# Performance work log

Measured on AMD Instinct MI355X. Metric: run time of the kernel, lower is better.

## Reference

```python
import jax, jax.numpy as jnp
import numpy as np

N, K, G = 4096, 4096, 128  # out_features, in_features, groupsize


def setup_inputs() -> dict:
    key = jax.random.key(0)
    k1, k2, k3, k4 = jax.random.split(key, 4)
    input = jax.random.normal(k1, (1, 2048, K), dtype=jnp.float32)
    # packed int4 weights: each byte holds two 4-bit codes (high nibble = even k, low = odd k)
    weight_packed = jax.random.randint(k2, (N, K // 2), 0, 256, dtype=jnp.int32)
    scales = jax.random.uniform(k3, (K // G, N), dtype=jnp.float32) * 0.02 + 1e-3
    zeros = jax.random.normal(k4, (K // G, N), dtype=jnp.float32) * 0.05
    scales_and_zeros = jnp.stack([scales, zeros], axis=-1)  # (K//G, N, 2)
    return {"input": input, "weight_packed": weight_packed,
            "scales_and_zeros": scales_and_zeros, "groupsize": G}


def reference(input, weight_packed, scales_and_zeros, groupsize):
    n, k_half = weight_packed.shape
    k = 2 * k_half
    g = k // groupsize
    # unpack two int4 codes per byte: high nibble first (even k index), then low nibble
    hi = (weight_packed >> 4) & 0xF
    lo = weight_packed & 0xF
    q = jnp.stack([hi, lo], axis=-1).reshape(n, k)  # (N, K), codes in [0,15]
    scales = scales_and_zeros[..., 0].T  # (N, G)
    zeros = scales_and_zeros[..., 1].T   # (N, G)
    # group-wise affine dequant: w = (q - 8) * scale + zero
    qg = q.reshape(n, g, groupsize).astype(jnp.float32)
    w = (qg - 8.0) * scales[:, :, None] + zeros[:, :, None]  # (N, G, gs)
    w = w.reshape(n, k)
    # out[..., n] = sum_k input[..., k] * w[n, k]
    return jnp.einsum('bsk,nk->bsn', input, w)
```

## Files before the change

kernel.cpp:

```cpp
#include <hip/hip_runtime.h>
#include <hip/hip_bf16.h>


using bf16x8 = __attribute__((ext_vector_type(8))) short;
using f32x16 = __attribute__((ext_vector_type(16))) float;

#define KK 4096
#define NN 4096
#define NT (KK / 64)

static __device__ __forceinline__ short f2bf(float f) {
    __hip_bfloat16 h = __float2bfloat16(f);
    return __builtin_bit_cast(short, h);
}

#define GLDS16(gptr, lptr) __builtin_amdgcn_global_load_lds( \
    (const __attribute__((address_space(1))) void*)(gptr),   \
    (__attribute__((address_space(3))) void*)(lptr), 16, 0, 0)

#define MFMA32 __builtin_amdgcn_mfma_f32_32x32x16_bf16

__global__ __launch_bounds__(256) void dequant_w(
    const int* __restrict__ W, const float* __restrict__ SZ,
    short* __restrict__ Wd)
{
    const int idx = blockIdx.x * 256 + threadIdx.x;
    const int n   = idx >> 9;
    const int q4  = idx & 511;
    const int kh0 = q4 << 2;
    const int g   = kh0 >> 6;
    const float2 sz = *(const float2*)(SZ + ((size_t)g * NN + n) * 2);
    const float scale = sz.x;
    const float zs    = sz.y - 8.0f * sz.x;
    int4 p = *(const int4*)(W + (size_t)n * (KK / 2) + kh0);
    int vals[4] = {p.x, p.y, p.z, p.w};
    bf16x8 r;
    #pragma unroll
    for (int j = 0; j < 4; ++j) {
        int v = vals[j];
        r[2 * j]     = f2bf((float)((v >> 4) & 0xF) * scale + zs);
        r[2 * j + 1] = f2bf((float)(v & 0xF) * scale + zs);
    }
    *(bf16x8*)&Wd[(size_t)n * KK + (kh0 << 1)] = r;
}

__global__ __launch_bounds__(256) void cvt_a(
    const float* __restrict__ A, short* __restrict__ Ab)
{
    const int idx = blockIdx.x * 256 + threadIdx.x;
    const float4* s = (const float4*)(A + (size_t)idx * 8);
    float4 u = s[0], v = s[1];
    bf16x8 r;
    r[0] = f2bf(u.x); r[1] = f2bf(u.y); r[2] = f2bf(u.z); r[3] = f2bf(u.w);
    r[4] = f2bf(v.x); r[5] = f2bf(v.y); r[6] = f2bf(v.z); r[7] = f2bf(v.w);
    *(bf16x8*)&Ab[(size_t)idx * 8] = r;
}

__global__ __launch_bounds__(512, 2) void gemm_pl(
    const short* __restrict__ Ab, const short* __restrict__ Bb,
    float* __restrict__ C)
{
    __shared__ short sA[3 * 256 * 64];
    __shared__ short sB[3 * 128 * 64];

    const int tid  = threadIdx.x;
    const int lane = tid & 63;
    const int wave = tid >> 6;
    const int wm   = wave >> 1;
    const int wn   = wave & 1;
    const int bm   = blockIdx.y * 256;
    const int bn   = blockIdx.x * 128;

    const int sl = lane >> 3;
    const int sc = (lane & 7) ^ sl;
    const short* aSt = Ab + (size_t)(bm + wave * 32 + sl) * KK + sc * 8;
    const short* bSt = Bb + (size_t)(bn + wave * 16 + sl) * KK + sc * 8;

    const int l31 = lane & 31;
    const int lx  = lane >> 5;
    const int l7  = lane & 7;
    const int px0 = ((0 + lx) ^ l7) * 8;
    const int px1 = ((2 + lx) ^ l7) * 8;
    const int px2 = ((4 + lx) ^ l7) * 8;
    const int px3 = ((6 + lx) ^ l7) * 8;
    const int aRd = (wm * 64 + l31) * 64;
    const int bRd = (wn * 64 + l31) * 64;

    f32x16 acc00 = {}, acc01 = {}, acc10 = {}, acc11 = {};
    bf16x8 pA00, pA01, pA10, pA11, pB00, pB01, pB10, pB11;
    bf16x8 qA00, qA01, qA10, qA11, qB00, qB01, qB10, qB11;

    #pragma unroll
    for (int l = 0; l < 4; ++l)
        GLDS16(aSt + (size_t)l * 8 * KK,      &sA[(wave * 32 + l * 8) * 64]);
    #pragma unroll
    for (int l = 0; l < 2; ++l)
        GLDS16(bSt + (size_t)l * 8 * KK,      &sB[(wave * 16 + l * 8) * 64]);
    #pragma unroll
    for (int l = 0; l < 4; ++l)
        GLDS16(aSt + (size_t)l * 8 * KK + 64, &sA[16384 + (wave * 32 + l * 8) * 64]);
    #pragma unroll
    for (int l = 0; l < 2; ++l)
        GLDS16(bSt + (size_t)l * 8 * KK + 64, &sB[8192 + (wave * 16 + l * 8) * 64]);
    asm volatile("s_waitcnt vmcnt(6)" ::: "memory");
    __builtin_amdgcn_s_barrier();

    pA00 = *(const bf16x8*)&sA[aRd + px0];
    pA01 = *(const bf16x8*)&sA[aRd + px1];
    pA10 = *(const bf16x8*)&sA[aRd + 2048 + px0];
    pA11 = *(const bf16x8*)&sA[aRd + 2048 + px1];
    pB00 = *(const bf16x8*)&sB[bRd + px0];
    pB01 = *(const bf16x8*)&sB[bRd + px1];
    pB10 = *(const bf16x8*)&sB[bRd + 2048 + px0];
    pB11 = *(const bf16x8*)&sB[bRd + 2048 + px1];
    asm volatile("s_waitcnt lgkmcnt(0)" ::: "memory");
    __builtin_amdgcn_sched_barrier(0);

    int cur = 0;
    for (int t = 0; t < NT; ++t) {
        const int nxt1 = (cur == 2) ? 0 : cur + 1;
        const int nxt2 = (nxt1 == 2) ? 0 : nxt1 + 1;
        const short* sAc = &sA[cur * 16384];
        const short* sBc = &sB[cur * 8192];
        const short* sA1 = &sA[nxt1 * 16384];
        const short* sB1 = &sB[nxt1 * 8192];
        short* sAn = &sA[nxt2 * 16384];
        short* sBn = &sB[nxt2 * 8192];
        const bool st = (t + 2 < NT);
        const int gk = (t + 2) * 64;

        qA00 = *(const bf16x8*)&sAc[aRd + px2];
        qA01 = *(const bf16x8*)&sAc[aRd + px3];
        qA10 = *(const bf16x8*)&sAc[aRd + 2048 + px2];
        qA11 = *(const bf16x8*)&sAc[aRd + 2048 + px3];
        qB00 = *(const bf16x8*)&sBc[bRd + px2];
        qB01 = *(const bf16x8*)&sBc[bRd + px3];
        qB10 = *(const bf16x8*)&sBc[bRd + 2048 + px2];
        qB11 = *(const bf16x8*)&sBc[bRd + 2048 + px3];
        if (st) {
            GLDS16(aSt + (size_t)0 * 8 * KK + gk, sAn + (wave * 32 + 0) * 64);
            GLDS16(aSt + (size_t)1 * 8 * KK + gk, sAn + (wave * 32 + 8) * 64);
            GLDS16(bSt + (size_t)0 * 8 * KK + gk, sBn + (wave * 16 + 0) * 64);
        }
        __builtin_amdgcn_sched_barrier(0);

        __builtin_amdgcn_s_setprio(1);
        acc00 = MFMA32(pA00, pB00, acc00, 0, 0, 0);
        acc00 = MFMA32(pA01, pB01, acc00, 0, 0, 0);
        acc01 = MFMA32(pA00, pB10, acc01, 0, 0, 0);
        acc01 = MFMA32(pA01, pB11, acc01, 0, 0, 0);
        acc10 = MFMA32(pA10, pB00, acc10, 0, 0, 0);
        acc10 = MFMA32(pA11, pB01, acc10, 0, 0, 0);
        acc11 = MFMA32(pA10, pB10, acc11, 0, 0, 0);
        acc11 = MFMA32(pA11, pB11, acc11, 0, 0, 0);
        __builtin_amdgcn_s_setprio(0);

        asm volatile("s_waitcnt lgkmcnt(0)" ::: "memory");
        __builtin_amdgcn_sched_barrier(0);
        if (t < NT - 2) {
            asm volatile("s_waitcnt vmcnt(3)" ::: "memory");
        } else {
            asm volatile("s_waitcnt vmcnt(0)" ::: "memory");
        }
        __builtin_amdgcn_s_barrier();

        if (t + 1 < NT) {
            pA00 = *(const bf16x8*)&sA1[aRd + px0];
            pA01 = *(const bf16x8*)&sA1[aRd + px1];
            pA10 = *(const bf16x8*)&sA1[aRd + 2048 + px0];
            pA11 = *(const bf16x8*)&sA1[aRd + 2048 + px1];
            pB00 = *(const bf16x8*)&sB1[bRd + px0];
            pB01 = *(const bf16x8*)&sB1[bRd + px1];
            pB10 = *(const bf16x8*)&sB1[bRd + 2048 + px0];
            pB11 = *(const bf16x8*)&sB1[bRd + 2048 + px1];
        }
        if (st) {
            GLDS16(aSt + (size_t)2 * 8 * KK + gk, sAn + (wave * 32 + 16) * 64);
            GLDS16(aSt + (size_t)3 * 8 * KK + gk, sAn + (wave * 32 + 24) * 64);
            GLDS16(bSt + (size_t)1 * 8 * KK + gk, sBn + (wave * 16 + 8) * 64);
        }
        __builtin_amdgcn_sched_barrier(0);

        __builtin_amdgcn_s_setprio(1);
        acc00 = MFMA32(qA00, qB00, acc00, 0, 0, 0);
        acc00 = MFMA32(qA01, qB01, acc00, 0, 0, 0);
        acc01 = MFMA32(qA00, qB10, acc01, 0, 0, 0);
        acc01 = MFMA32(qA01, qB11, acc01, 0, 0, 0);
        acc10 = MFMA32(qA10, qB00, acc10, 0, 0, 0);
        acc10 = MFMA32(qA11, qB01, acc10, 0, 0, 0);
        acc11 = MFMA32(qA10, qB10, acc11, 0, 0, 0);
        acc11 = MFMA32(qA11, qB11, acc11, 0, 0, 0);
        __builtin_amdgcn_s_setprio(0);

        asm volatile("s_waitcnt lgkmcnt(0)" ::: "memory");
        __builtin_amdgcn_sched_barrier(0);

        cur = nxt1;
    }

    {
        const int crow = lx * 4;
        float* Cp = C + (size_t)(bm + wm * 64) * NN + bn + wn * 64;
        #pragma unroll
        for (int m = 0; m < 2; ++m) {
            #pragma unroll
            for (int qr = 0; qr < 4; ++qr) {
                #pragma unroll
                for (int j = 0; j < 4; ++j) {
                    const int row = m * 32 + crow + j + 8 * qr;
                    float* dst = Cp + (size_t)row * NN + l31;
                    if (m == 0) {
                        dst[0]  = acc00[qr * 4 + j];
                        dst[32] = acc01[qr * 4 + j];
                    } else {
                        dst[0]  = acc10[qr * 4 + j];
                        dst[32] = acc11[qr * 4 + j];
                    }
                }
            }
        }
    }
}

using f32x4 = __attribute__((ext_vector_type(4))) float;
#define LDKF 72
__global__ __launch_bounds__(256) void wq4_gemm_fused(
    const float* __restrict__ A, const int* __restrict__ W,
    const float* __restrict__ SZ, float* __restrict__ C, int M)
{
    __shared__ short sA[128 * LDKF];
    __shared__ short sB[128 * LDKF];
    const int tid = threadIdx.x, lane = tid & 63, wave = tid >> 6;
    const int wr = (wave >> 1) << 6, wc = (wave & 1) << 6;
    const int bm = blockIdx.y * 128, bn = blockIdx.x * 128;
    const int ar = tid >> 2, ac = (tid & 3) << 4;
    const int br = tid >> 1, bh = (tid & 1) << 4;
    const float* Arow0 = A + (size_t)(bm + ar) * KK + ac;
    const float* Arow1 = A + (size_t)(bm + 64 + ar) * KK + ac;
    const int*   Wrow  = W + (size_t)(bn + br) * (KK / 2) + bh;
    const float* SZrow = SZ + (size_t)(bn + br) * 2;
    f32x4 acc[4][4] = {};
    for (int k0 = 0; k0 < KK; k0 += 64) {
        {
            const float4* s0 = (const float4*)(Arow0 + k0);
            const float4* s1 = (const float4*)(Arow1 + k0);
            float4 a0 = s0[0], a1 = s0[1], a2 = s0[2], a3 = s0[3];
            float4 b0 = s1[0], b1 = s1[1], b2 = s1[2], b3 = s1[3];
            auto cvt8 = [](float4 u, float4 v) -> bf16x8 {
                bf16x8 r;
                r[0] = f2bf(u.x); r[1] = f2bf(u.y); r[2] = f2bf(u.z); r[3] = f2bf(u.w);
                r[4] = f2bf(v.x); r[5] = f2bf(v.y); r[6] = f2bf(v.z); r[7] = f2bf(v.w);
                return r;
            };
            *(bf16x8*)&sA[ar * LDKF + ac]            = cvt8(a0, a1);
            *(bf16x8*)&sA[ar * LDKF + ac + 8]        = cvt8(a2, a3);
            *(bf16x8*)&sA[(64 + ar) * LDKF + ac]     = cvt8(b0, b1);
            *(bf16x8*)&sA[(64 + ar) * LDKF + ac + 8] = cvt8(b2, b3);
        }
        {
            const int g = k0 >> 7;
            const float2 sz = *(const float2*)(SZrow + (size_t)g * NN * 2);
            const float scale = sz.x, zs = sz.y - 8.0f * sz.x;
            const int4* src = (const int4*)(Wrow + (k0 >> 1));
            #pragma unroll
            for (int i = 0; i < 4; ++i) {
                int4 p = src[i];
                int vals[4] = {p.x, p.y, p.z, p.w};
                bf16x8 r;
                #pragma unroll
                for (int j = 0; j < 4; ++j) {
                    int v = vals[j];
                    r[2 * j]     = f2bf((float)((v >> 4) & 0xF) * scale + zs);
                    r[2 * j + 1] = f2bf((float)(v & 0xF) * scale + zs);
                }
                *(bf16x8*)&sB[br * LDKF + (bh << 1) + (i << 3)] = r;
            }
        }
        __syncthreads();
        #pragma unroll
        for (int ks = 0; ks < 2; ++ks) {
            const int col = (ks << 5) + ((lane >> 4) << 3);
            bf16x8 af[4], bfr[4];
            #pragma unroll
            for (int m = 0; m < 4; ++m)
                af[m] = *(const bf16x8*)&sA[(wr + m * 16 + (lane & 15)) * LDKF + col];
            #pragma unroll
            for (int n = 0; n < 4; ++n)
                bfr[n] = *(const bf16x8*)&sB[(wc + n * 16 + (lane & 15)) * LDKF + col];
            #pragma unroll
            for (int m = 0; m < 4; ++m)
                #pragma unroll
                for (int n = 0; n < 4; ++n)
                    acc[m][n] = __builtin_amdgcn_mfma_f32_16x16x32_bf16(
                        af[m], bfr[n], acc[m][n], 0, 0, 0);
        }
        __syncthreads();
    }
    float* Cp = C + (size_t)(bm + wr) * NN + bn + wc;
    const int cr = (lane >> 4) << 2, cc = lane & 15;
    #pragma unroll
    for (int m = 0; m < 4; ++m)
        #pragma unroll
        for (int j = 0; j < 4; ++j) {
            float* dst = Cp + (size_t)(m * 16 + cr + j) * NN + cc;
            #pragma unroll
            for (int n = 0; n < 4; ++n) dst[n * 16] = acc[m][n][j];
        }
}

extern "C" void kernel_launch(void* const* d_in, const int* in_sizes, int n_in,
                              void* d_out, int out_size, void* d_ws, size_t ws_size,
                              hipStream_t stream) {
    const float* A  = (const float*)d_in[0];
    const int*   W  = (const int*)d_in[1];
    const float* SZ = (const float*)d_in[2];
    float* C = (float*)d_out;

    const int M = in_sizes[0] / KK;

    const size_t wd_elems = (size_t)NN * KK;
    const size_t ab_elems = (size_t)M * KK;
    const size_t need = (wd_elems + ab_elems) * sizeof(short);

    if (ws_size >= need && (M % 256) == 0) {
        short* Wd = (short*)d_ws;
        short* Ab = Wd + wd_elems;
        dequant_w<<<NN * (KK / 8) / 256, 256, 0, stream>>>(W, SZ, Wd);
        cvt_a<<<(int)(ab_elems / 8 / 256), 256, 0, stream>>>(A, Ab);
        dim3 grid(NN / 128, M / 256);
        gemm_pl<<<grid, dim3(512), 0, stream>>>(Ab, Wd, C);
    } else {
        dim3 grid(NN / 128, M / 128);
        wq4_gemm_fused<<<grid, dim3(256), 0, stream>>>(A, W, SZ, C, M);
    }
}
```

Baseline: 93.78 us.

## Replace 256x128 triple-buffered GEMM with 128x128 double-buffered 4-wave kernel

The bf16 GEMM drops from 512-thread blocks with 256x128 tiles and a three-stage LDS ring to 256-thread blocks with 128x128 tiles and two LDS buffers. All global-to-LDS loads for the next K step are issued at the top of each iteration, and the loop waits for them fully before the barrier. The aim is lower LDS use and more, smaller blocks for better occupancy and wave spread (512 blocks instead of 256). The cost is less prefetch depth, since the loop now drains vmcnt(0) every step, and less reuse of each loaded A/B tile per MFMA.

```diff
diff --git a/kernel.cpp b/kernel.cpp
--- a/kernel.cpp
+++ b/kernel.cpp
@@ -4,6 +4,7 @@
 
 using bf16x8 = __attribute__((ext_vector_type(8))) short;
 using f32x16 = __attribute__((ext_vector_type(16))) float;
+using f32x4  = __attribute__((ext_vector_type(4))) float;
 
 #define KK 4096
 #define NN 4096
@@ -19,6 +20,7 @@
     (__attribute__((address_space(3))) void*)(lptr), 16, 0, 0)
 
 #define MFMA32 __builtin_amdgcn_mfma_f32_32x32x16_bf16
+#define SBAR() __builtin_amdgcn_sched_barrier(0)
 
 __global__ __launch_bounds__(256) void dequant_w(
     const int* __restrict__ W, const float* __restrict__ SZ,
@@ -56,25 +58,25 @@
     *(bf16x8*)&Ab[(size_t)idx * 8] = r;
 }
 
-__global__ __launch_bounds__(512, 2) void gemm_pl(
+__global__ __launch_bounds__(256, 2) void gemm_2b(
     const short* __restrict__ Ab, const short* __restrict__ Bb,
     float* __restrict__ C)
 {
-    __shared__ short sA[3 * 256 * 64];
-    __shared__ short sB[3 * 128 * 64];
+    __shared__ short sA[2 * 128 * 64];
+    __shared__ short sB[2 * 128 * 64];
 
     const int tid  = threadIdx.x;
     const int lane = tid & 63;
     const int wave = tid >> 6;
     const int wm   = wave >> 1;
     const int wn   = wave & 1;
-    const int bm   = blockIdx.y * 256;
+    const int bm   = blockIdx.y * 128;
     const int bn   = blockIdx.x * 128;
 
     const int sl = lane >> 3;
     const int sc = (lane & 7) ^ sl;
     const short* aSt = Ab + (size_t)(bm + wave * 32 + sl) * KK + sc * 8;
-    const short* bSt = Bb + (size_t)(bn + wave * 16 + sl) * KK + sc * 8;
+    const short* bSt = Bb + (size_t)(bn + wave * 32 + sl) * KK + sc * 8;
 
     const int l31 = lane & 31;
     const int lx  = lane >> 5;
@@ -92,17 +94,11 @@
 
     #pragma unroll
     for (int l = 0; l < 4; ++l)
-        GLDS16(aSt + (size_t)l * 8 * KK,      &sA[(wave * 32 + l * 8) * 64]);
-    #pragma unroll
-    for (int l = 0; l < 2; ++l)
-        GLDS16(bSt + (size_t)l * 8 * KK,      &sB[(wave * 16 + l * 8) * 64]);
+        GLDS16(aSt + (size_t)l * 8 * KK, &sA[(wave * 32 + l * 8) * 64]);
     #pragma unroll
     for (int l = 0; l < 4; ++l)
-        GLDS16(aSt + (size_t)l * 8 * KK + 64, &sA[16384 + (wave * 32 + l * 8) * 64]);
-    #pragma unroll
-    for (int l = 0; l < 2; ++l)
-        GLDS16(bSt + (size_t)l * 8 * KK + 64, &sB[8192 + (wave * 16 + l * 8) * 64]);
-    asm volatile("s_waitcnt vmcnt(6)" ::: "memory");
+        GLDS16(bSt + (size_t)l * 8 * KK, &sB[(wave * 32 + l * 8) * 64]);
+    asm volatile("s_waitcnt vmcnt(0)" ::: "memory");
     __builtin_amdgcn_s_barrier();
 
     pA00 = *(const bf16x8*)&sA[aRd + px0];
@@ -114,20 +110,27 @@
     pB10 = *(const bf16x8*)&sB[bRd + 2048 + px0];
     pB11 = *(const bf16x8*)&sB[bRd + 2048 + px1];
     asm volatile("s_waitcnt lgkmcnt(0)" ::: "memory");
-    __builtin_amdgcn_sched_barrier(0);
+    SBAR();
 
     int cur = 0;
     for (int t = 0; t < NT; ++t) {
-        const int nxt1 = (cur == 2) ? 0 : cur + 1;
-        const int nxt2 = (nxt1 == 2) ? 0 : nxt1 + 1;
-        const short* sAc = &sA[cur * 16384];
+        const short* sAc = &sA[cur * 8192];
         const short* sBc = &sB[cur * 8192];
-        const short* sA1 = &sA[nxt1 * 16384];
-        const short* sB1 = &sB[nxt1 * 8192];
-        short* sAn = &sA[nxt2 * 16384];
-        short* sBn = &sB[nxt2 * 8192];
-        const bool st = (t + 2 < NT);
-        const int gk = (t + 2) * 64;
+        short* sAn = &sA[(cur ^ 1) * 8192];
+        short* sBn = &sB[(cur ^ 1) * 8192];
+        const bool st = (t + 1 < NT);
+        const int gk = (t + 1) * 64;
+
+        if (st) {
+            GLDS16(aSt + (size_t)0 * 8 * KK + gk, sAn + (wave * 32 + 0) * 64);
+            GLDS16(aSt + (size_t)1 * 8 * KK + gk, sAn + (wave * 32 + 8) * 64);
+            GLDS16(aSt + (size_t)2 * 8 * KK + gk, sAn + (wave * 32 + 16) * 64);
+            GLDS16(aSt + (size_t)3 * 8 * KK + gk, sAn + (wave * 32 + 24) * 64);
+            GLDS16(bSt + (size_t)0 * 8 * KK + gk, sBn + (wave * 32 + 0) * 64);
+            GLDS16(bSt + (size_t)1 * 8 * KK + gk, sBn + (wave * 32 + 8) * 64);
+            GLDS16(bSt + (size_t)2 * 8 * KK + gk, sBn + (wave * 32 + 16) * 64);
+            GLDS16(bSt + (size_t)3 * 8 * KK + gk, sBn + (wave * 32 + 24) * 64);
+        }
 
         qA00 = *(const bf16x8*)&sAc[aRd + px2];
         qA01 = *(const bf16x8*)&sAc[aRd + px3];
@@ -137,12 +140,7 @@
         qB01 = *(const bf16x8*)&sBc[bRd + px3];
         qB10 = *(const bf16x8*)&sBc[bRd + 2048 + px2];
         qB11 = *(const bf16x8*)&sBc[bRd + 2048 + px3];
-        if (st) {
-            GLDS16(aSt + (size_t)0 * 8 * KK + gk, sAn + (wave * 32 + 0) * 64);
-            GLDS16(aSt + (size_t)1 * 8 * KK + gk, sAn + (wave * 32 + 8) * 64);
-            GLDS16(bSt + (size_t)0 * 8 * KK + gk, sBn + (wave * 16 + 0) * 64);
-        }
-        __builtin_amdgcn_sched_barrier(0);
+        SBAR();
 
         __builtin_amdgcn_s_setprio(1);
         acc00 = MFMA32(pA00, pB00, acc00, 0, 0, 0);
@@ -156,30 +154,21 @@
         __builtin_amdgcn_s_setprio(0);
 
         asm volatile("s_waitcnt lgkmcnt(0)" ::: "memory");
-        __builtin_amdgcn_sched_barrier(0);
-        if (t < NT - 2) {
-            asm volatile("s_waitcnt vmcnt(3)" ::: "memory");
-        } else {
-            asm volatile("s_waitcnt vmcnt(0)" ::: "memory");
-        }
+        SBAR();
+        asm volatile("s_waitcnt vmcnt(0)" ::: "memory");
         __builtin_amdgcn_s_barrier();
 
-        if (t + 1 < NT) {
-            pA00 = *(const bf16x8*)&sA1[aRd + px0];
-            pA01 = *(const bf16x8*)&sA1[aRd + px1];
-            pA10 = *(const bf16x8*)&sA1[aRd + 2048 + px0];
-            pA11 = *(const bf16x8*)&sA1[aRd + 2048 + px1];
-            pB00 = *(const bf16x8*)&sB1[bRd + px0];
-            pB01 = *(const bf16x8*)&sB1[bRd + px1];
-            pB10 = *(const bf16x8*)&sB1[bRd + 2048 + px0];
-            pB11 = *(const bf16x8*)&sB1[bRd + 2048 + px1];
-        }
         if (st) {
-            GLDS16(aSt + (size_t)2 * 8 * KK + gk, sAn + (wave * 32 + 16) * 64);
-            GLDS16(aSt + (size_t)3 * 8 * KK + gk, sAn + (wave * 32 + 24) * 64);
-            GLDS16(bSt + (size_t)1 * 8 * KK + gk, sBn + (wave * 16 + 8) * 64);
-        }
-        __builtin_amdgcn_sched_barrier(0);
+            pA00 = *(const bf16x8*)&sAn[aRd + px0];
+            pA01 = *(const bf16x8*)&sAn[aRd + px1];
+            pA10 = *(const bf16x8*)&sAn[aRd + 2048 + px0];
+            pA11 = *(const bf16x8*)&sAn[aRd + 2048 + px1];
+            pB00 = *(const bf16x8*)&sBn[bRd + px0];
+            pB01 = *(const bf16x8*)&sBn[bRd + px1];
+            pB10 = *(const bf16x8*)&sBn[bRd + 2048 + px0];
+            pB11 = *(const bf16x8*)&sBn[bRd + 2048 + px1];
+        }
+        SBAR();
 
         __builtin_amdgcn_s_setprio(1);
         acc00 = MFMA32(qA00, qB00, acc00, 0, 0, 0);
@@ -193,9 +182,9 @@
         __builtin_amdgcn_s_setprio(0);
 
         asm volatile("s_waitcnt lgkmcnt(0)" ::: "memory");
-        __builtin_amdgcn_sched_barrier(0);
-
-        cur = nxt1;
+        SBAR();
+
+        cur ^= 1;
     }
 
     {
@@ -222,7 +211,6 @@
     }
 }
 
-using f32x4 = __attribute__((ext_vector_type(4))) float;
 #define LDKF 72
 __global__ __launch_bounds__(256) void wq4_gemm_fused(
     const float* __restrict__ A, const int* __restrict__ W,
@@ -318,17 +306,17 @@
 
     const int M = in_sizes[0] / KK;
 
-    const size_t wd_elems = (size_t)NN * KK;
-    const size_t ab_elems = (size_t)M * KK;
-    const size_t need = (wd_elems + ab_elems) * sizeof(short);
-
-    if (ws_size >= need && (M % 256) == 0) {
+    const size_t wd_e = (size_t)NN * KK;
+    const size_t ab_e = (size_t)M * KK;
+    const size_t need = (wd_e + ab_e) * sizeof(short);
+
+    if (ws_size >= need && (M % 128) == 0) {
         short* Wd = (short*)d_ws;
-        short* Ab = Wd + wd_elems;
+        short* Ab = Wd + wd_e;
         dequant_w<<<NN * (KK / 8) / 256, 256, 0, stream>>>(W, SZ, Wd);
-        cvt_a<<<(int)(ab_elems / 8 / 256), 256, 0, stream>>>(A, Ab);
-        dim3 grid(NN / 128, M / 256);
-        gemm_pl<<<grid, dim3(512), 0, stream>>>(Ab, Wd, C);
+        cvt_a<<<(int)(ab_e / 8 / 256), 256, 0, stream>>>(A, Ab);
+        dim3 grid(NN / 128, M / 128);
+        gemm_2b<<<grid, dim3(256), 0, stream>>>(Ab, Wd, C);
     } else {
         dim3 grid(NN / 128, M / 128);
         wq4_gemm_fused<<<grid, dim3(256), 0, stream>>>(A, W, SZ, C, M);
```

After: 104.1 us. 1.11x slower.
